# Kernel optimization log

Measured on AMD Instinct MI355X. Metric: run time of the kernel, lower is better.

Reference implementation:

```python
import jax, jax.numpy as jnp
from jax import lax
import numpy as np

EMB = 64
HID = 128
CELL = 0.5
NX = 6
NY = 6
OBS_LEN = 2048
TOT_LEN = 4096
N_NEIGH = 4096


def setup_inputs() -> dict:
    key = jax.random.key(0)
    ks = jax.random.split(key, 8)
    observed = jax.random.normal(ks[0], (OBS_LEN, 1, 2), dtype=jnp.float32) * 3.0
    other_paths = jax.random.normal(ks[1], (TOT_LEN, N_NEIGH, 2), dtype=jnp.float32) * 30.0
    s = 0.05
    in_dim = EMB + NX * NY  # 64 + 36
    W_emb = jax.random.normal(ks[2], (EMB, 2), dtype=jnp.float32) * s
    b_emb = jnp.zeros((EMB,), jnp.float32)
    W_ih = jax.random.normal(ks[3], (4 * HID, in_dim), dtype=jnp.float32) * s
    b_ih = jnp.zeros((4 * HID,), jnp.float32)
    W_hh = jax.random.normal(ks[4], (4 * HID, HID), dtype=jnp.float32) * s
    b_hh = jnp.zeros((4 * HID,), jnp.float32)
    W_out = jax.random.normal(ks[5], (5, HID), dtype=jnp.float32) * s
    b_out = jnp.zeros((5,), jnp.float32)
    return {"observed": observed, "other_paths": other_paths,
            "W_emb": W_emb, "b_emb": b_emb, "W_ih": W_ih, "b_ih": b_ih,
            "W_hh": W_hh, "b_hh": b_hh, "W_out": W_out, "b_out": b_out}


def _occupancy(center, others):
    # center: (2,) position of primary ped at the new time step
    # others: (N, 2) neighbor positions at the new time step
    half = NX / 2 * CELL  # 1.5
    gx = jnp.linspace(-half, half, NX + 1) + center[0]  # (7,)
    gy = jnp.linspace(-half, half, NY + 1) + center[1]
    x = others[:, 0]
    y = others[:, 1]
    in_x = (gx[:-1, None] < x[None, :]) & (x[None, :] < gx[1:, None])  # (6, N)
    in_y = (gy[:-1, None] < y[None, :]) & (y[None, :] < gy[1:, None])  # (6, N)
    occ = jnp.any(in_x[:, None, :] & in_y[None, :, :], axis=-1)  # (6, 6), x outer / y inner
    return occ.reshape(NX * NY).astype(jnp.float32)  # (36,)


def reference(observed, other_paths, W_emb, b_emb, W_ih, b_ih, W_hh, b_hh, W_out, b_out):
    O = observed.shape[0]
    T = other_paths.shape[0]
    H = W_hh.shape[1]

    def embed(d):  # (1, 2) -> (1, EMB)
        return jax.nn.relu(d @ W_emb.T + b_emb)

    def cell(x, h, c):  # PyTorch LSTMCell gate order: i, f, g, o
        g = x @ W_ih.T + b_ih + h @ W_hh.T + b_hh
        i, f, gg, o = jnp.split(g, 4, axis=-1)
        c = jax.nn.sigmoid(f) * c + jax.nn.sigmoid(i) * jnp.tanh(gg)
        h = jax.nn.sigmoid(o) * jnp.tanh(c)
        return h, c

    # Phase 1: condition on observed positions (O-1 steps)
    def step1(carry, xs):
        h, c = carry
        obs1, obs2, oth2 = xs  # (1,2), (1,2), (N,2)
        occ = _occupancy(obs2[0], oth2)[None, :]  # (1, 36)
        emb = jnp.concatenate([embed(obs2 - obs1), occ], axis=1)
        h, c = cell(emb, h, c)
        normal = h @ W_out.T + b_out  # (1, 5)
        pos = obs2 + normal[:, :2]
        return (h, c), (normal, pos)

    h0 = jnp.zeros((1, H), observed.dtype)
    c0 = jnp.zeros((1, H), observed.dtype)
    (h, c), (normals1, positions1) = lax.scan(
        step1, (h0, c0), (observed[:-1], observed[1:], other_paths[1:O]))

    # occupancy binned against future neighbor ground truth other_paths[O:T-1]
    def step2(carry, oth2):
        h, c, pp, pc = carry
        occ = _occupancy(pc[0], oth2)[None, :]
        emb = jnp.concatenate([embed(lax.stop_gradient(pc - pp)), occ], axis=1)
        h, c = cell(emb, h, c)
        normal = h @ W_out.T + b_out
        newp = pc + normal[:, :2]
        return (h, c, pc, newp), normal

    carry0 = (h, c, positions1[-2], positions1[-1])
    _, normals2 = lax.scan(step2, carry0, other_paths[O:T - 1])

    # training-mode output: stacked normals, shape (T-2, 1, 5)
    return jnp.concatenate([normals1, normals2], axis=0)
```

## Files before the change

kernel.cpp:

```cpp
#include <hip/hip_runtime.h>

#define NN    4096
#define OBSN  2048
#define S1    2047
#define S2    2047
#define HID   128
#define INDIM 100
#define TOTT  (S1 + S2)
#define WTP   520

typedef float v2f __attribute__((ext_vector_type(2)));
typedef float v4f __attribute__((ext_vector_type(4)));

__device__ __forceinline__ void bar() {
    asm volatile("s_waitcnt lgkmcnt(0)\n\ts_barrier" ::: "memory");
}

__device__ __forceinline__ float sigm(float x) {
    return 1.0f / (1.0f + __expf(-x));
}
__device__ __forceinline__ float tanh_(float x) {
    float e = __expf(2.0f * x);
    return 1.0f - 2.0f / (e + 1.0f);
}

#define DPPF(x, ctrl) __int_as_float(__builtin_amdgcn_update_dpp(0, __float_as_int(x), (ctrl), 0xF, 0xF, true))

__device__ __forceinline__ float qsum(float x) {
    x += DPPF(x, 0xB1);
    x += DPPF(x, 0x4E);
    return x;
}
__device__ __forceinline__ float usum(float x) {
    x += DPPF(DPPF(x, 0x141), 0x1B);
    x += DPPF(DPPF(x, 0x140), 0x141);
    x += __int_as_float(__builtin_amdgcn_ds_swizzle(__float_as_int(x), 0x401F));
    auto r = __builtin_amdgcn_permlane32_swap(__float_as_int(x), __float_as_int(x), false, false);
    return __int_as_float(r[0]) + __int_as_float(r[1]);
}

__device__ __forceinline__ unsigned long long classify(float x, float y,
                                                       const float* bx, const float* by) {
    int a = 0, b = 0, c = 0, d = 0;
#pragma unroll
    for (int j = 0; j < 7; j++) {
        a += bx[j] < x;
        b += x < bx[j];
        c += by[j] < y;
        d += y < by[j];
    }
    if (a >= 1 && a <= 6 && (a + b) == 7 && c >= 1 && c <= 6 && (c + d) == 7)
        return 1ull << ((a - 1) * 6 + (c - 1));
    return 0ull;
}

__device__ __forceinline__ float hsum8(const float* p8) {
    const v4f a = ((const v4f*)p8)[0];
    const v4f b = ((const v4f*)p8)[1];
    return ((a.x + a.y) + (a.z + a.w)) + ((b.x + b.y) + (b.z + b.w));
}

__global__ __launch_bounds__(256) void k_occ1(const float* __restrict__ obs,
                                              const float* __restrict__ oth,
                                              unsigned long long* __restrict__ occm) {
    const int t = blockIdx.x;
    const int slice = t + 1;
    const float cx = obs[slice * 2 + 0];
    const float cy = obs[slice * 2 + 1];
    const float CST[7] = {-1.5f, -1.0f, -0.5f, 0.0f, 0.5f, 1.0f, 1.5f};
    float bx[7], by[7];
#pragma unroll
    for (int j = 0; j < 7; j++) { bx[j] = CST[j] + cx; by[j] = CST[j] + cy; }

    const float2* p = (const float2*)(oth + (size_t)slice * NN * 2);
    unsigned long long m = 0ull;
#pragma unroll 4
    for (int i = 0; i < 16; i++) {
        float2 q = p[i * 256 + threadIdx.x];
        if (q.x > bx[0] && q.x < bx[6] && q.y > by[0] && q.y < by[6])
            m |= classify(q.x, q.y, bx, by);
    }
#pragma unroll
    for (int off = 32; off > 0; off >>= 1) m |= __shfl_down(m, off);
    __shared__ unsigned long long sm[4];
    if ((threadIdx.x & 63) == 0) sm[threadIdx.x >> 6] = m;
    __syncthreads();
    if (threadIdx.x == 0) occm[t] = sm[0] | sm[1] | sm[2] | sm[3];
}

__global__ void k_tr(const float* __restrict__ W_ih, float* __restrict__ WT) {
    WT[blockIdx.x * 512 + threadIdx.x] = W_ih[threadIdx.x * INDIM + 64 + blockIdx.x];
}

__global__ __launch_bounds__(256) void k_g1(const float* __restrict__ obs,
                                            const float* __restrict__ W_emb,
                                            const float* __restrict__ b_emb,
                                            const float* __restrict__ W_ih,
                                            const float* __restrict__ b_ih,
                                            const float* __restrict__ b_hh,
                                            const unsigned long long* __restrict__ occm,
                                            float* __restrict__ G1) {
    const int t = blockIdx.x;
    const int tid = threadIdx.x;
    __shared__ __align__(16) float e[64];
    const float d0 = obs[(t + 1) * 2 + 0] - obs[t * 2 + 0];
    const float d1 = obs[(t + 1) * 2 + 1] - obs[t * 2 + 1];
    if (tid < 64) {
        float v = W_emb[tid * 2 + 0] * d0 + W_emb[tid * 2 + 1] * d1 + b_emb[tid];
        e[tid] = v > 0.0f ? v : 0.0f;
    }
    __syncthreads();
    const unsigned long long m = occm[t];
#pragma unroll
    for (int rr = 0; rr < 2; rr++) {
        const int r = tid + rr * 256;
        const float* wr = W_ih + r * INDIM;
        float s = b_ih[r] + b_hh[r];
        float4 acc = {0.f, 0.f, 0.f, 0.f};
        const float4* w4 = (const float4*)wr;
        const float4* e4 = (const float4*)e;
#pragma unroll
        for (int q = 0; q < 16; q++) {
            float4 w = w4[q], ev = e4[q];
            acc.x += w.x * ev.x; acc.y += w.y * ev.y;
            acc.z += w.z * ev.z; acc.w += w.w * ev.w;
        }
        s += (acc.x + acc.y) + (acc.z + acc.w);
        unsigned long long mm = m;
        while (mm) {
            int j = __ffsll((long long)mm) - 1;
            mm &= mm - 1;
            s += wr[64 + j];
        }
        G1[t * 512 + r] = s;
    }
}

__global__ __launch_bounds__(512, 2) void k_seq(const float* __restrict__ obs,
                                                const float* __restrict__ oth,
                                                const float* __restrict__ W_emb,
                                                const float* __restrict__ b_emb,
                                                const float* __restrict__ W_ih,
                                                const float* __restrict__ b_ih,
                                                const float* __restrict__ W_hh,
                                                const float* __restrict__ b_hh,
                                                const float* __restrict__ W_out,
                                                const float* __restrict__ b_out,
                                                const float* __restrict__ G1,
                                                const float* __restrict__ WT,
                                                float* __restrict__ hist) {
    const int tid  = threadIdx.x;
    const int wv   = tid >> 6;
    const int lane = tid & 63;
    const int u    = wv * 16 + (lane >> 2);
    const int k    = lane & 3;

    v2f whh[4][16];
#pragma unroll
    for (int g = 0; g < 4; g++) {
        const v2f* src = (const v2f*)(W_hh + (u + 128 * g) * HID + 32 * k);
#pragma unroll
        for (int j = 0; j < 16; j++) whh[g][j] = src[j];
    }

    const float won0 = W_out[u];
    const float won1 = W_out[HID + u];
    const float bo0 = b_out[0], bo1 = b_out[1];
    float we0 = 0.f, we1 = 0.f, be = 0.f;
    if (tid < 64) { we0 = W_emb[tid * 2]; we1 = W_emb[tid * 2 + 1]; be = b_emb[tid]; }
    const float obsA0 = obs[(S1 - 1) * 2], obsA1 = obs[(S1 - 1) * 2 + 1];
    const float obsB0 = obs[S1 * 2],       obsB1 = obs[S1 * 2 + 1];

    __shared__ __align__(16) float WTl[36 * WTP];
    __shared__ __align__(16) float hbuf[2][HID];
    __shared__ __align__(16) float e_lds[64];
    __shared__ __align__(16) float redn[2][8];
    __shared__ unsigned int mword[4];

    for (int i = tid; i < 36 * 512; i += 512)
        WTl[(i >> 9) * WTP + (i & 511)] = WT[i];
    if (tid < 4) mword[tid] = 0u;
    if (tid < HID) hbuf[0][tid] = 0.0f;
    float c = 0.0f;
    float p1x = 0.f, p1y = 0.f, p2x = 0.f, p2y = 0.f;
    int p = 0;
    __syncthreads();

    v4f g1v;
    {
        const float* gp = G1 + u;
        g1v.x = gp[0]; g1v.y = gp[128]; g1v.z = gp[256]; g1v.w = gp[384];
    }

    for (int t = 0; t < S1; ++t) {
        const v4f cur = g1v;
        const int tn = (t + 1 < S1) ? t + 1 : t;
        {
            const float* gp = G1 + tn * 512 + u;
            g1v.x = gp[0]; g1v.y = gp[128]; g1v.z = gp[256]; g1v.w = gp[384];
        }

        v2f a0 = {0.f, 0.f}, a1 = {0.f, 0.f}, a2 = {0.f, 0.f}, a3 = {0.f, 0.f};
        const v4f* h4 = ((const v4f*)hbuf[p]) + k * 8;
#pragma unroll
        for (int q = 0; q < 8; q++) {
            const v4f hv = h4[q];
            const v2f hl = hv.xy, hh2 = hv.zw;
            a0 = whh[0][2*q] * hl + a0;  a0 = whh[0][2*q+1] * hh2 + a0;
            a1 = whh[1][2*q] * hl + a1;  a1 = whh[1][2*q+1] * hh2 + a1;
            a2 = whh[2][2*q] * hl + a2;  a2 = whh[2][2*q+1] * hh2 + a2;
            a3 = whh[3][2*q] * hl + a3;  a3 = whh[3][2*q+1] * hh2 + a3;
        }
        float pg0 = (a0.x + a0.y) + ((k == 0) ? cur.x : 0.0f);
        float pg1 = (a1.x + a1.y) + ((k == 0) ? cur.y : 0.0f);
        float pg2 = (a2.x + a2.y) + ((k == 0) ? cur.z : 0.0f);
        float pg3 = (a3.x + a3.y) + ((k == 0) ? cur.w : 0.0f);
        pg0 = qsum(pg0); pg1 = qsum(pg1); pg2 = qsum(pg2); pg3 = qsum(pg3);

        const float gi = sigm(pg0), gf = sigm(pg1);
        const float gG = tanh_(pg2), go = sigm(pg3);
        c = gf * c + gi * gG;
        const float h = go * tanh_(c);
        if (k == 0) {
            hbuf[p ^ 1][u] = h;
            hist[(size_t)t * HID + u] = h;
        }

        if (t >= S1 - 2) {
            float pd = (k == 0 ? won0 : (k == 1 ? won1 : 0.0f)) * h;
            pd = usum(pd);
            if (lane < 2) redn[lane][wv] = pd;
            bar();
            const float n0 = hsum8(redn[0]) + bo0;
            const float n1 = hsum8(redn[1]) + bo1;
            if (t == S1 - 2) { p1x = obsA0 + n0; p1y = obsA1 + n1; }
            else             { p2x = obsB0 + n0; p2y = obsB1 + n1; }
        }
        bar();
        p ^= 1;
    }

    v2f wie[4][8];
#pragma unroll
    for (int g = 0; g < 4; g++) {
        const v2f* src = (const v2f*)(W_ih + (u + 128 * g) * INDIM + 16 * k);
#pragma unroll
        for (int j = 0; j < 8; j++) wie[g][j] = src[j];
    }
    float biasg[4];
#pragma unroll
    for (int g = 0; g < 4; g++) biasg[g] = b_ih[u + 128 * g] + b_hh[u + 128 * g];

    float pcx = p2x, pcy = p2y;
    float dx = p2x - p1x, dy = p2y - p1y;

    v4f nb[4];
    {
        const v4f* s0 = (const v4f*)(oth + (size_t)OBSN * NN * 2);
#pragma unroll
        for (int i = 0; i < 4; i++) nb[i] = s0[i * 512 + tid];
    }
    if (tid < 64) {
        float v = we0 * dx + we1 * dy + be;
        e_lds[tid] = v > 0.0f ? v : 0.0f;
    }
    const float CST[7] = {-1.5f, -1.0f, -0.5f, 0.0f, 0.5f, 1.0f, 1.5f};
    int sl = 0;

    for (int s = 0; s < S2; ++s) {
        float bx[7], by[7];
#pragma unroll
        for (int j = 0; j < 7; j++) { bx[j] = CST[j] + pcx; by[j] = CST[j] + pcy; }

        unsigned long long m = 0ull;
#pragma unroll
        for (int i = 0; i < 4; i++) {
            const v4f q = nb[i];
            if (q.x > bx[0] && q.x < bx[6] && q.y > by[0] && q.y < by[6])
                m |= classify(q.x, q.y, bx, by);
            if (q.z > bx[0] && q.z < bx[6] && q.w > by[0] && q.w < by[6])
                m |= classify(q.z, q.w, bx, by);
        }
        {
            const int sn = (s + 1 < S2) ? s + 1 : s;
            const v4f* pf = (const v4f*)(oth + (size_t)(OBSN + sn) * NN * 2);
#pragma unroll
            for (int i = 0; i < 4; i++) nb[i] = pf[i * 512 + tid];
        }
        if (m) {
            const unsigned int lo = (unsigned int)m;
            const unsigned int hi = (unsigned int)(m >> 32);
            if (lo) atomicOr(&mword[sl * 2 + 0], lo);
            if (hi) atomicOr(&mword[sl * 2 + 1], hi);
        }
        bar();

        const unsigned long long mm =
            (unsigned long long)mword[sl * 2] |
            ((unsigned long long)mword[sl * 2 + 1] << 32);
        if (tid == 0) { mword[(sl ^ 1) * 2] = 0u; mword[(sl ^ 1) * 2 + 1] = 0u; }

        float og0 = (k == 0) ? biasg[0] : 0.0f;
        float og1 = (k == 0) ? biasg[1] : 0.0f;
        float og2 = (k == 0) ? biasg[2] : 0.0f;
        float og3 = (k == 0) ? biasg[3] : 0.0f;
        {
            unsigned long long mm2 = mm;
            int idx = 0;
            while (mm2) {
                const int j = __ffsll((long long)mm2) - 1;
                mm2 &= mm2 - 1;
                if ((idx & 3) == k) {
                    const float* wc = WTl + j * WTP + u;
                    og0 += wc[0];
                    og1 += wc[128];
                    og2 += wc[256];
                    og3 += wc[384];
                }
                idx++;
            }
        }

        v2f a0 = {0.f, 0.f}, a1 = {0.f, 0.f}, a2 = {0.f, 0.f}, a3 = {0.f, 0.f};
        {
            const v4f* e4 = ((const v4f*)e_lds) + k * 4;
#pragma unroll
            for (int q = 0; q < 4; q++) {
                const v4f ev = e4[q];
                const v2f el = ev.xy, eh = ev.zw;
                a0 = wie[0][2*q] * el + a0;  a0 = wie[0][2*q+1] * eh + a0;
                a1 = wie[1][2*q] * el + a1;  a1 = wie[1][2*q+1] * eh + a1;
                a2 = wie[2][2*q] * el + a2;  a2 = wie[2][2*q+1] * eh + a2;
                a3 = wie[3][2*q] * el + a3;  a3 = wie[3][2*q+1] * eh + a3;
            }
            const v4f* h4 = ((const v4f*)hbuf[p]) + k * 8;
#pragma unroll
            for (int q = 0; q < 8; q++) {
                const v4f hv = h4[q];
                const v2f hl = hv.xy, hh2 = hv.zw;
                a0 = whh[0][2*q] * hl + a0;  a0 = whh[0][2*q+1] * hh2 + a0;
                a1 = whh[1][2*q] * hl + a1;  a1 = whh[1][2*q+1] * hh2 + a1;
                a2 = whh[2][2*q] * hl + a2;  a2 = whh[2][2*q+1] * hh2 + a2;
                a3 = whh[3][2*q] * hl + a3;  a3 = whh[3][2*q+1] * hh2 + a3;
            }
        }
        float pg0 = og0 + (a0.x + a0.y);
        float pg1 = og1 + (a1.x + a1.y);
        float pg2 = og2 + (a2.x + a2.y);
        float pg3 = og3 + (a3.x + a3.y);
        pg0 = qsum(pg0); pg1 = qsum(pg1); pg2 = qsum(pg2); pg3 = qsum(pg3);

        const float gi = sigm(pg0), gf = sigm(pg1);
        const float gG = tanh_(pg2), go = sigm(pg3);
        c = gf * c + gi * gG;
        const float h = go * tanh_(c);
        if (k == 0) {
            hbuf[p ^ 1][u] = h;
            hist[(size_t)(S1 + s) * HID + u] = h;
        }

        float pd = (k == 0 ? won0 : (k == 1 ? won1 : 0.0f)) * h;
        pd = usum(pd);
        if (lane < 2) redn[lane][wv] = pd;
        bar();

        const float n0 = hsum8(redn[0]) + bo0;
        const float n1 = hsum8(redn[1]) + bo1;
        dx = n0; dy = n1;
        pcx += n0; pcy += n1;
        if (tid < 64) {
            float v = we0 * dx + we1 * dy + be;
            e_lds[tid] = v > 0.0f ? v : 0.0f;
        }
        p ^= 1; sl ^= 1;
    }
}

__global__ __launch_bounds__(64) void k_out(const float* __restrict__ hist,
                                            const float* __restrict__ W_out,
                                            const float* __restrict__ b_out,
                                            float* __restrict__ out) {
    const int t = blockIdx.x;
    const int l = threadIdx.x;
    const float h0 = hist[(size_t)t * HID + l];
    const float h1 = hist[(size_t)t * HID + 64 + l];
#pragma unroll
    for (int d = 0; d < 5; ++d) {
        float pz = W_out[d * HID + l] * h0 + W_out[d * HID + 64 + l] * h1;
#pragma unroll
        for (int off = 1; off < 64; off <<= 1) pz += __shfl_xor(pz, off);
        if (l == 0) out[t * 5 + d] = pz + b_out[d];
    }
}

extern "C" void kernel_launch(void* const* d_in, const int* in_sizes, int n_in,
                              void* d_out, int out_size, void* d_ws, size_t ws_size,
                              hipStream_t stream) {
    const float* obs   = (const float*)d_in[0];
    const float* oth   = (const float*)d_in[1];
    const float* W_emb = (const float*)d_in[2];
    const float* b_emb = (const float*)d_in[3];
    const float* W_ih  = (const float*)d_in[4];
    const float* b_ih  = (const float*)d_in[5];
    const float* W_hh  = (const float*)d_in[6];
    const float* b_hh  = (const float*)d_in[7];
    const float* W_out = (const float*)d_in[8];
    const float* b_out = (const float*)d_in[9];
    float* out = (float*)d_out;

    unsigned long long* occm = (unsigned long long*)d_ws;
    float* G1   = (float*)((char*)d_ws + 16384);
    float* WT   = (float*)((char*)d_ws + 16384 + (size_t)S1 * 512 * 4);
    float* hist = (float*)((char*)d_ws + 16384 + (size_t)S1 * 512 * 4 + (size_t)36 * 512 * 4);

    k_occ1<<<S1, 256, 0, stream>>>(obs, oth, occm);
    k_tr<<<36, 512, 0, stream>>>(W_ih, WT);
    k_g1<<<S1, 256, 0, stream>>>(obs, W_emb, b_emb, W_ih, b_ih, b_hh, occm, G1);
    k_seq<<<1, 512, 0, stream>>>(obs, oth, W_emb, b_emb, W_ih, b_ih, W_hh, b_hh,
                                 W_out, b_out, G1, WT, hist);
    k_out<<<TOTT, 64, 0, stream>>>(hist, W_out, b_out, out);
}
```

Measured before the change: 7.668 ms.

## Pad LDS buffers, deepen G1 prefetch, branchless occupancy gather in recurrent loop

Pads the hidden-state and embedding LDS buffers so each of the four k-groups reads from a different bank offset, which is meant to cut bank conflicts. The phase-1 G1 prefetch now looks two steps ahead instead of one. The occupancy mask is made wave-uniform with readfirstlane, and the first 12 set bits are gathered branchlessly from a zero-padded 37th row of the weight table. The loop keeps only a tail for any further bits, and the W_hh/W_ih dot products move ahead of the mask gather to overlap LDS latency. The neighbor box test is simplified to a Chebyshev-distance check, and the next-step neighbor prefetch is issued after the atomics.

New measurement: 11.22 ms. 1.46x slower.

```diff
diff --git a/kernel.cpp b/kernel.cpp
--- a/kernel.cpp
+++ b/kernel.cpp
@@ -8,6 +8,9 @@
 #define INDIM 100
 #define TOTT  (S1 + S2)
 #define WTP   520
+
+#define HIDX(c) ((c) + 4 * ((c) >> 5))
+#define EIDX(c) ((c) + 4 * ((c) >> 4))
 
 typedef float v2f __attribute__((ext_vector_type(2)));
 typedef float v4f __attribute__((ext_vector_type(4)));
@@ -171,37 +174,41 @@
     const float obsA0 = obs[(S1 - 1) * 2], obsA1 = obs[(S1 - 1) * 2 + 1];
     const float obsB0 = obs[S1 * 2],       obsB1 = obs[S1 * 2 + 1];
 
-    __shared__ __align__(16) float WTl[36 * WTP];
-    __shared__ __align__(16) float hbuf[2][HID];
-    __shared__ __align__(16) float e_lds[64];
+    __shared__ __align__(16) float WTl[37 * WTP];
+    __shared__ __align__(16) float hbufP[2][144];
+    __shared__ __align__(16) float e_ldsP[80];
     __shared__ __align__(16) float redn[2][8];
     __shared__ unsigned int mword[4];
 
     for (int i = tid; i < 36 * 512; i += 512)
         WTl[(i >> 9) * WTP + (i & 511)] = WT[i];
+    WTl[36 * WTP + tid] = 0.0f;
     if (tid < 4) mword[tid] = 0u;
-    if (tid < HID) hbuf[0][tid] = 0.0f;
+    if (tid < HID) hbufP[0][HIDX(tid)] = 0.0f;
     float c = 0.0f;
     float p1x = 0.f, p1y = 0.f, p2x = 0.f, p2y = 0.f;
     int p = 0;
     __syncthreads();
 
-    v4f g1v;
+    v4f g1_cur, g1_nxt;
     {
         const float* gp = G1 + u;
-        g1v.x = gp[0]; g1v.y = gp[128]; g1v.z = gp[256]; g1v.w = gp[384];
+        g1_cur.x = gp[0]; g1_cur.y = gp[128]; g1_cur.z = gp[256]; g1_cur.w = gp[384];
+        const float* gq = G1 + 512 + u;
+        g1_nxt.x = gq[0]; g1_nxt.y = gq[128]; g1_nxt.z = gq[256]; g1_nxt.w = gq[384];
     }
 
     for (int t = 0; t < S1; ++t) {
-        const v4f cur = g1v;
-        const int tn = (t + 1 < S1) ? t + 1 : t;
+        const v4f cur = g1_cur;
+        v4f g1_fut;
         {
-            const float* gp = G1 + tn * 512 + u;
-            g1v.x = gp[0]; g1v.y = gp[128]; g1v.z = gp[256]; g1v.w = gp[384];
+            const int tf = (t + 2 < S1) ? t + 2 : S1 - 1;
+            const float* gp = G1 + tf * 512 + u;
+            g1_fut.x = gp[0]; g1_fut.y = gp[128]; g1_fut.z = gp[256]; g1_fut.w = gp[384];
         }
 
         v2f a0 = {0.f, 0.f}, a1 = {0.f, 0.f}, a2 = {0.f, 0.f}, a3 = {0.f, 0.f};
-        const v4f* h4 = ((const v4f*)hbuf[p]) + k * 8;
+        const v4f* h4 = (const v4f*)(&hbufP[p][36 * k]);
 #pragma unroll
         for (int q = 0; q < 8; q++) {
             const v4f hv = h4[q];
@@ -222,7 +229,7 @@
         c = gf * c + gi * gG;
         const float h = go * tanh_(c);
         if (k == 0) {
-            hbuf[p ^ 1][u] = h;
+            hbufP[p ^ 1][HIDX(u)] = h;
             hist[(size_t)t * HID + u] = h;
         }
 
@@ -238,6 +245,7 @@
         }
         bar();
         p ^= 1;
+        g1_cur = g1_nxt; g1_nxt = g1_fut;
     }
 
     v2f wie[4][8];
@@ -262,7 +270,7 @@
     }
     if (tid < 64) {
         float v = we0 * dx + we1 * dy + be;
-        e_lds[tid] = v > 0.0f ? v : 0.0f;
+        e_ldsP[EIDX(tid)] = v > 0.0f ? v : 0.0f;
     }
     const float CST[7] = {-1.5f, -1.0f, -0.5f, 0.0f, 0.5f, 1.0f, 1.5f};
     int sl = 0;
@@ -276,16 +284,10 @@
 #pragma unroll
         for (int i = 0; i < 4; i++) {
             const v4f q = nb[i];
-            if (q.x > bx[0] && q.x < bx[6] && q.y > by[0] && q.y < by[6])
-                m |= classify(q.x, q.y, bx, by);
-            if (q.z > bx[0] && q.z < bx[6] && q.w > by[0] && q.w < by[6])
-                m |= classify(q.z, q.w, bx, by);
-        }
-        {
-            const int sn = (s + 1 < S2) ? s + 1 : s;
-            const v4f* pf = (const v4f*)(oth + (size_t)(OBSN + sn) * NN * 2);
-#pragma unroll
-            for (int i = 0; i < 4; i++) nb[i] = pf[i * 512 + tid];
+            const float tA = fmaxf(fabsf(q.x - pcx), fabsf(q.y - pcy));
+            const float tB = fmaxf(fabsf(q.z - pcx), fabsf(q.w - pcy));
+            if (tA < 1.6f) m |= classify(q.x, q.y, bx, by);
+            if (tB < 1.6f) m |= classify(q.z, q.w, bx, by);
         }
         if (m) {
             const unsigned int lo = (unsigned int)m;
@@ -293,20 +295,71 @@
             if (lo) atomicOr(&mword[sl * 2 + 0], lo);
             if (hi) atomicOr(&mword[sl * 2 + 1], hi);
         }
+        {
+            const int sn = (s + 1 < S2) ? s + 1 : s;
+            const v4f* pf = (const v4f*)(oth + (size_t)(OBSN + sn) * NN * 2);
+#pragma unroll
+            for (int i = 0; i < 4; i++) nb[i] = pf[i * 512 + tid];
+        }
         bar();
 
-        const unsigned long long mm =
-            (unsigned long long)mword[sl * 2] |
-            ((unsigned long long)mword[sl * 2 + 1] << 32);
+        const unsigned int mlo_v = mword[sl * 2 + 0];
+        const unsigned int mhi_v = mword[sl * 2 + 1];
         if (tid == 0) { mword[(sl ^ 1) * 2] = 0u; mword[(sl ^ 1) * 2 + 1] = 0u; }
+
+        unsigned long long um =
+            ((unsigned long long)(unsigned int)__builtin_amdgcn_readfirstlane((int)mhi_v) << 32) |
+            (unsigned long long)(unsigned int)__builtin_amdgcn_readfirstlane((int)mlo_v);
+        int e0, e1, e2, e3, e4i, e5, e6, e7, e8, e9, e10, e11;
+#define EXT(v) v = um ? (int)(__ffsll((long long)um) - 1) : 36; um &= um - 1;
+        EXT(e0) EXT(e1) EXT(e2) EXT(e3) EXT(e4i) EXT(e5)
+        EXT(e6) EXT(e7) EXT(e8) EXT(e9) EXT(e10) EXT(e11)
+#undef EXT
+        const int j0 = (k == 0) ? e0 : (k == 1) ? e1  : (k == 2) ? e2  : e3;
+        const int j1 = (k == 0) ? e4i: (k == 1) ? e5  : (k == 2) ? e6  : e7;
+        const int j2 = (k == 0) ? e8 : (k == 1) ? e9  : (k == 2) ? e10 : e11;
+        const float* w0 = WTl + j0 * WTP + u;
+        const float* w1 = WTl + j1 * WTP + u;
+        const float* w2 = WTl + j2 * WTP + u;
+        const float c00 = w0[0], c01 = w0[128], c02 = w0[256], c03 = w0[384];
+        const float c10 = w1[0], c11 = w1[128], c12 = w1[256], c13 = w1[384];
+        const float c20 = w2[0], c21 = w2[128], c22 = w2[256], c23 = w2[384];
+
+        v2f a0 = {0.f, 0.f}, a1 = {0.f, 0.f}, a2 = {0.f, 0.f}, a3 = {0.f, 0.f};
+        {
+            const v4f* e4 = (const v4f*)(&e_ldsP[20 * k]);
+#pragma unroll
+            for (int q = 0; q < 4; q++) {
+                const v4f ev = e4[q];
+                const v2f el = ev.xy, eh = ev.zw;
+                a0 = wie[0][2*q] * el + a0;  a0 = wie[0][2*q+1] * eh + a0;
+                a1 = wie[1][2*q] * el + a1;  a1 = wie[1][2*q+1] * eh + a1;
+                a2 = wie[2][2*q] * el + a2;  a2 = wie[2][2*q+1] * eh + a2;
+                a3 = wie[3][2*q] * el + a3;  a3 = wie[3][2*q+1] * eh + a3;
+            }
+            const v4f* h4 = (const v4f*)(&hbufP[p][36 * k]);
+#pragma unroll
+            for (int q = 0; q < 8; q++) {
+                const v4f hv = h4[q];
+                const v2f hl = hv.xy, hh2 = hv.zw;
+                a0 = whh[0][2*q] * hl + a0;  a0 = whh[0][2*q+1] * hh2 + a0;
+                a1 = whh[1][2*q] * hl + a1;  a1 = whh[1][2*q+1] * hh2 + a1;
+                a2 = whh[2][2*q] * hl + a2;  a2 = whh[2][2*q+1] * hh2 + a2;
+                a3 = whh[3][2*q] * hl + a3;  a3 = whh[3][2*q+1] * hh2 + a3;
+            }
+        }
 
         float og0 = (k == 0) ? biasg[0] : 0.0f;
         float og1 = (k == 0) ? biasg[1] : 0.0f;
         float og2 = (k == 0) ? biasg[2] : 0.0f;
         float og3 = (k == 0) ? biasg[3] : 0.0f;
-        {
-            unsigned long long mm2 = mm;
-            int idx = 0;
+        og0 += c00; og0 += c10; og0 += c20;
+        og1 += c01; og1 += c11; og1 += c21;
+        og2 += c02; og2 += c12; og2 += c22;
+        og3 += c03; og3 += c13; og3 += c23;
+        if (um) {
+            unsigned long long mm2 = um;
+            int idx = 12;
             while (mm2) {
                 const int j = __ffsll((long long)mm2) - 1;
                 mm2 &= mm2 - 1;
@@ -321,29 +374,6 @@
             }
         }
 
-        v2f a0 = {0.f, 0.f}, a1 = {0.f, 0.f}, a2 = {0.f, 0.f}, a3 = {0.f, 0.f};
-        {
-            const v4f* e4 = ((const v4f*)e_lds) + k * 4;
-#pragma unroll
-            for (int q = 0; q < 4; q++) {
-                const v4f ev = e4[q];
-                const v2f el = ev.xy, eh = ev.zw;
-                a0 = wie[0][2*q] * el + a0;  a0 = wie[0][2*q+1] * eh + a0;
-                a1 = wie[1][2*q] * el + a1;  a1 = wie[1][2*q+1] * eh + a1;
-                a2 = wie[2][2*q] * el + a2;  a2 = wie[2][2*q+1] * eh + a2;
-                a3 = wie[3][2*q] * el + a3;  a3 = wie[3][2*q+1] * eh + a3;
-            }
-            const v4f* h4 = ((const v4f*)hbuf[p]) + k * 8;
-#pragma unroll
-            for (int q = 0; q < 8; q++) {
-                const v4f hv = h4[q];
-                const v2f hl = hv.xy, hh2 = hv.zw;
-                a0 = whh[0][2*q] * hl + a0;  a0 = whh[0][2*q+1] * hh2 + a0;
-                a1 = whh[1][2*q] * hl + a1;  a1 = whh[1][2*q+1] * hh2 + a1;
-                a2 = whh[2][2*q] * hl + a2;  a2 = whh[2][2*q+1] * hh2 + a2;
-                a3 = whh[3][2*q] * hl + a3;  a3 = whh[3][2*q+1] * hh2 + a3;
-            }
-        }
         float pg0 = og0 + (a0.x + a0.y);
         float pg1 = og1 + (a1.x + a1.y);
         float pg2 = og2 + (a2.x + a2.y);
@@ -355,7 +385,7 @@
         c = gf * c + gi * gG;
         const float h = go * tanh_(c);
         if (k == 0) {
-            hbuf[p ^ 1][u] = h;
+            hbufP[p ^ 1][HIDX(u)] = h;
             hist[(size_t)(S1 + s) * HID + u] = h;
         }
 
@@ -370,7 +400,7 @@
         pcx += n0; pcy += n1;
         if (tid < 64) {
             float v = we0 * dx + we1 * dy + be;
-            e_lds[tid] = v > 0.0f ? v : 0.0f;
+            e_ldsP[EIDX(tid)] = v > 0.0f ? v : 0.0f;
         }
         p ^= 1; sl ^= 1;
     }
```
